# Performance work log

Measured on AMD Instinct MI355X. Metric: run time of the kernel, lower is better.

## Reference

```python
import jax, jax.numpy as jnp
import numpy as np

H = 1024
K = 4  # window_size (causal conv kernel)
HIGHWAY_BIAS = -2.0
SCALE_X = float(np.sqrt(1.0 + np.exp(2.0 * HIGHWAY_BIAS)))  # SRU rescale factor


def _layernorm(x, w, b, eps=1e-5):
    m = jnp.mean(x, axis=-1, keepdims=True)
    v = jnp.mean((x - m) ** 2, axis=-1, keepdims=True)
    return (x - m) * jax.lax.rsqrt(v + eps) * w + b


def _rmsnorm(x, w, eps=1e-6):
    v = jnp.mean(x ** 2, axis=-1, keepdims=True)
    return w * (x * jax.lax.rsqrt(v + eps))


def setup_inputs() -> dict:
    key = jax.random.key(0)
    ks = jax.random.split(key, 12)
    B, L = 8, 4096
    s = 1.0 / np.sqrt(H)
    inp = {
        "x": jax.random.normal(ks[0], (B, L, H), jnp.float32),
        # causal conv1d (full, not depthwise): (out_ch, in_ch, K)
        "conv_w": jax.random.normal(ks[1], (H, H, K), jnp.float32) * (1.0 / np.sqrt(H * K)),
        "conv_b": jnp.zeros((H,), jnp.float32),
        # SRU cell params (k=3 since input_size == hidden_size)
        "sru_ln_w": jnp.ones((H,), jnp.float32),
        "sru_ln_b": jnp.zeros((H,), jnp.float32),
        "sru_W": jax.random.normal(ks[2], (H, 3 * H), jnp.float32) * s,
        "sru_vf": jax.random.normal(ks[3], (H,), jnp.float32) * s,
        "sru_vr": jax.random.normal(ks[4], (H,), jnp.float32) * s,
        "sru_bf": jnp.full((H,), HIGHWAY_BIAS, jnp.float32),
        "sru_br": jnp.zeros((H,), jnp.float32),
        # lambda gate + RMSNorm
        "lambda_w": jax.random.normal(ks[5], (H,), jnp.float32),
        "rms_w": jnp.ones((H,), jnp.float32),
        # FFN token mixer (internal = 2H)
        "ln1_w": jnp.ones((H,), jnp.float32),
        "ln1_b": jnp.zeros((H,), jnp.float32),
        "lin1_w": jax.random.normal(ks[6], (H, 2 * H), jnp.float32) * s,
        "ln2_w": jnp.ones((2 * H,), jnp.float32),
        "ln2_b": jnp.zeros((2 * H,), jnp.float32),
        "lin2_w": jax.random.normal(ks[7], (2 * H, H), jnp.float32) * (1.0 / np.sqrt(2 * H)),
        "lin2_b": jnp.zeros((H,), jnp.float32),
    }
    return inp


def _forward(x, conv_w, conv_b, sru_ln_w, sru_ln_b, sru_W, sru_vf, sru_vr,
             sru_bf, sru_br, lambda_w, rms_w, ln1_w, ln1_b, lin1_w,
             ln2_w, ln2_b, lin2_w, lin2_b):
    B, L, _ = x.shape
    # --- causal conv1d: left-pad K-1, valid conv ---
    xt = jnp.transpose(x, (0, 2, 1))                      # (B, H, L)
    xt = jnp.pad(xt, ((0, 0), (0, 0), (K - 1, 0)))        # (B, H, L+K-1)
    cnn = jax.lax.conv_general_dilated(
        xt, conv_w, window_strides=(1,), padding="VALID",
        dimension_numbers=("NCH", "OIH", "NCH"))          # (B, H, L)
    cnn = cnn + conv_b[None, :, None]
    cnn = jnp.transpose(cnn, (2, 0, 1))                   # (L, B, H)  time-major

    # --- SRU cell (layer_norm=True, use_tanh, rescale) ---
    xn = _layernorm(cnn, sru_ln_w, sru_ln_b)              # (L, B, H)
    U = xn @ sru_W                                        # (L, B, 3H)
    u0, u1, u2 = jnp.split(U, 3, axis=-1)
    xres = xn * SCALE_X

    def step(c, inputs):
        u0t, u1t, u2t, xrt = inputs
        f = jax.nn.sigmoid(u1t + c * sru_vf + sru_bf)
        c_new = f * c + (1.0 - f) * u0t
        r = jax.nn.sigmoid(u2t + c * sru_vr + sru_br)
        h = r * jnp.tanh(c_new) + (1.0 - r) * xrt
        return c_new, h

    c0 = jnp.zeros((B, x.shape[-1]), x.dtype)
    _, hs = jax.lax.scan(step, c0, (u0, u1, u2, xres))    # hs: (L, B, H)

    # --- lambda-gated blend + RMSNorm ---
    out = lambda_w * cnn + (1.0 - lambda_w) * hs          # (L, B, H)
    out = jnp.transpose(out, (1, 0, 2))                   # (B, L, H)
    out = _rmsnorm(out, rms_w)

    # --- block: gate by input, then FFN residual ---
    out = out * x
    t = _layernorm(out, ln1_w, ln1_b)
    t = jax.nn.gelu(t, approximate=False) @ lin1_w        # (B, L, 2H)
    t = _layernorm(t, ln2_w, ln2_b)
    t = jax.nn.gelu(t, approximate=False) @ lin2_w + lin2_b
    return t + out


def reference(x, conv_w, conv_b, sru_ln_w, sru_ln_b, sru_W, sru_vf, sru_vr,
              sru_bf, sru_br, lambda_w, rms_w, ln1_w, ln1_b, lin1_w,
              ln2_w, ln2_b, lin2_w, lin2_b):
    return _forward(x, conv_w, conv_b, sru_ln_w, sru_ln_b, sru_W, sru_vf,
                    sru_vr, sru_bf, sru_br, lambda_w, rms_w, ln1_w, ln1_b,
                    lin1_w, ln2_w, ln2_b, lin2_w, lin2_b)
```

## Files before the change

### kernel.cpp

```cpp
#include <hip/hip_runtime.h>

typedef unsigned short u16;
typedef short bf16x8 __attribute__((ext_vector_type(8)));
typedef float f32x4 __attribute__((ext_vector_type(4)));

#define NTOK 32768
#define LC 512
#define NCH 8
#define MC 8192
#define NFC 4

#define OFF_XB     0ull
#define OFF_CNNB   67108864ull
#define OFF_XNB    134217728ull
#define OFF_U4C    201326592ull
#define OFF_WCT    234881024ull
#define OFF_WSRUT  243269632ull
#define OFF_W1T    249561088ull
#define OFF_W2T    253755392ull
#define OFF_CARRY  257949696ull
#define OFF_P      257982464ull
#define OFF_SCALE  258048000ull
#define OFF_FLAG   258179072ull
#define OFF_ZERO   258179328ull
#define WS_REQ     258183168ull

#define P_CONVB 0
#define P_LNW   1024
#define P_LNB   2048
#define P_VF    3072
#define P_VR    4096
#define P_BF    5120
#define P_BR    6144
#define P_LAM   7168
#define P_RMS   8192
#define P_LN1W  9216
#define P_LN1B  10240
#define P_LIN2B 11264
#define P_LN2W  12288
#define P_LN2B  14336

__device__ __forceinline__ float b2f(u16 u) {
    union { unsigned int i; float f; } v; v.i = ((unsigned int)u) << 16; return v.f;
}
__device__ __forceinline__ u16 f2b(float f) {
    union { float f; unsigned int i; } v; v.f = f;
    unsigned int r = v.i + 0x7fffu + ((v.i >> 16) & 1u);
    return (u16)(r >> 16);
}
__device__ __forceinline__ float ldp(const void* p, size_t i, int fl) {
    return fl ? ((const float*)p)[i] : b2f(((const u16*)p)[i]);
}
__device__ __forceinline__ float gelu_exact(float a) {
    return 0.5f * a * (1.0f + erff(a * 0.70710678118654752f));
}

typedef const __attribute__((address_space(1))) void gas_void;
typedef __attribute__((address_space(3))) void las_void;
__device__ __forceinline__ void gl16(const u16* g, u16* l) {
    __builtin_amdgcn_global_load_lds((gas_void*)g, (las_void*)l, 16, 0, 0);
}

__device__ __forceinline__ int kswz(int row) { return (row + (row >> 3)) & 3; }

__global__ __launch_bounds__(256) void k_fill(float* out, float v) {
    size_t i = ((size_t)blockIdx.x * 256 + threadIdx.x) * 4;
    float4 o; o.x = v; o.y = v; o.z = v; o.w = v;
    *(float4*)(out + i) = o;
}

__global__ void k_detect(const u16* __restrict__ x, int* __restrict__ flag) {
    __shared__ int cnt[4];
    int tid = threadIdx.x;
    int c = 0;
    for (int i = 0; i < 16; ++i) {
        float f = b2f(x[2 * (tid * 16 + i)]);
        if (f != f || fabsf(f) > 1e6f) c++;
    }
    #pragma unroll
    for (int m = 32; m; m >>= 1) c += __shfl_xor(c, m, 64);
    if ((tid & 63) == 0) cnt[tid >> 6] = c;
    __syncthreads();
    if (tid == 0) flag[0] = (cnt[0] + cnt[1] + cnt[2] + cnt[3] > 100) ? 1 : 0;
}

__global__ __launch_bounds__(256) void k_params(const int* __restrict__ flag,
        const void* conv_b, const void* lnw, const void* lnb,
        const void* vf, const void* vr, const void* bf, const void* br,
        const void* lam, const void* rms, const void* ln1w, const void* ln1b,
        const void* lin2b, const void* ln2w, const void* ln2b,
        float* __restrict__ P, float* __restrict__ Z) {
    if (blockIdx.x == 0 && threadIdx.x < 32) Z[threadIdx.x] = 0.0f;
    int idx = blockIdx.x * 256 + threadIdx.x;
    int fl = flag[0];
    int vec = idx >> 10, off = idx & 1023;
    const void* src; size_t so = off;
    switch (vec) {
        case 0: src = conv_b; break;
        case 1: src = lnw; break;
        case 2: src = lnb; break;
        case 3: src = vf; break;
        case 4: src = vr; break;
        case 5: src = bf; break;
        case 6: src = br; break;
        case 7: src = lam; break;
        case 8: src = rms; break;
        case 9: src = ln1w; break;
        case 10: src = ln1b; break;
        case 11: src = lin2b; break;
        case 12: case 13: src = ln2w; so = idx - P_LN2W; break;
        default: src = ln2b; so = idx - P_LN2B; break;
    }
    P[idx] = ldp(src, so, fl);
}

__global__ __launch_bounds__(256) void k_x2b(const int* __restrict__ flag,
                                             const void* __restrict__ x, u16* __restrict__ xb) {
    size_t i = (size_t)blockIdx.x * 256 + threadIdx.x;
    int fl = flag[0];
    ushort4 o;
    if (fl) {
        float4 v = ((const float4*)x)[i];
        o.x = f2b(v.x); o.y = f2b(v.y); o.z = f2b(v.z); o.w = f2b(v.w);
    } else {
        o = ((const ushort4*)x)[i];
    }
    ((ushort4*)xb)[i] = o;
}

__global__ __launch_bounds__(256) void k_conv_reorder(const int* __restrict__ flag,
                                                      const void* __restrict__ w, u16* __restrict__ out) {
    int o = blockIdx.x, fl = flag[0];
    for (int kk = threadIdx.x; kk < 4096; kk += 256) {
        int k = kk >> 10, i = kk & 1023;
        out[(size_t)o * 4096 + kk] = f2b(ldp(w, (size_t)o * 4096 + i * 4 + k, fl));
    }
}

__global__ __launch_bounds__(256) void k_transpose(const int* __restrict__ flag,
                                                   const void* __restrict__ in, u16* __restrict__ out,
                                                   int R, int C) {
    int n = blockIdx.x, fl = flag[0];
    for (int r = threadIdx.x; r < R; r += 256)
        out[(size_t)n * R + r] = f2b(ldp(in, (size_t)r * C + n, fl));
}

template<int MODE, int EPI>
__global__ __launch_bounds__(256) void k_gemm(const u16* __restrict__ A, const u16* __restrict__ Bt,
                                              int N, int K, int nn, int l0, int tok0,
                                              const float* __restrict__ P,
                                              const u16* __restrict__ blend,
                                              const void* __restrict__ xorig,
                                              const float* __restrict__ scale,
                                              const int* __restrict__ flag,
                                              const u16* __restrict__ zb,
                                              void* __restrict__ outp) {
    __shared__ __align__(16) u16 As[128 * 32];
    __shared__ __align__(16) u16 Bs[128 * 32];
    const int tid = threadIdx.x;
    const int lane = tid & 63, wid = tid >> 6;
    const int wm = wid >> 1, wn = wid & 1;

    const int nwg = gridDim.x, bid = blockIdx.x;
    const int q = nwg >> 3, r = nwg & 7;
    const int xcd = bid & 7, idx = bid >> 3;
    const int swz = idx + (xcd < r ? xcd * (q + 1) : r * (q + 1) + (xcd - r) * q);
    const int mi = swz / nn, ni = swz - mi * nn;
    const int m0 = mi << 7, n0 = ni << 7;

    const u16* pa[2]; const u16* pb[2]; int kmin[2];
    u16 *la[2], *lb[2];
    #pragma unroll
    for (int j = 0; j < 2; ++j) {
        int s = tid + j * 256;
        int row = s >> 2;
        int kg = ((s & 3) ^ kswz(row)) << 3;
        la[j] = As + ((s & ~63) << 3);
        lb[j] = Bs + ((s & ~63) << 3);
        pb[j] = Bt + (size_t)(n0 + row) * K + kg;
        kmin[j] = 0;
        if (MODE == 1) {
            int t = m0 + row, b = t >> 12, l = t & 4095;
            pa[j] = A + (((size_t)(b << 12) + (size_t)(l - 3)) << 10) + kg;
            kmin[j] = (3 - l) << 10;
        } else if (MODE == 2) {
            int rg = m0 + row;
            int token = ((rg >> 9) << 12) + l0 + (rg & 511);
            pa[j] = A + ((size_t)token << 10) + kg;
        } else {
            pa[j] = A + (size_t)(m0 + row) * K + kg;
        }
    }

    f32x4 acc[4][4];
    #pragma unroll
    for (int a = 0; a < 4; ++a)
        #pragma unroll
        for (int b = 0; b < 4; ++b)
            #pragma unroll
            for (int rr = 0; rr < 4; ++rr) acc[a][b][rr] = 0.0f;

    int ra[4], rb[4];
    #pragma unroll
    for (int sm = 0; sm < 4; ++sm) {
        int rowa = wm * 64 + sm * 16 + (lane & 15);
        int rowb = wn * 64 + sm * 16 + (lane & 15);
        ra[sm] = (rowa << 5) + ((((lane >> 4) ^ kswz(rowa)) & 3) << 3);
        rb[sm] = (rowb << 5) + ((((lane >> 4) ^ kswz(rowb)) & 3) << 3);
    }

    const int nkb = K >> 5;
    for (int kb = 0; kb < nkb; ++kb) {
        const int k0 = kb << 5;
        __syncthreads();
        #pragma unroll
        for (int j = 0; j < 2; ++j) {
            const u16* ga = pa[j] + k0;
            if (MODE == 1) ga = (k0 < kmin[j]) ? zb : ga;
            gl16(ga, la[j]);
            gl16(pb[j] + k0, lb[j]);
        }
        __syncthreads();

        bf16x8 af[4], bfr[4];
        #pragma unroll
        for (int sm = 0; sm < 4; ++sm) af[sm] = *(const bf16x8*)(As + ra[sm]);
        #pragma unroll
        for (int sn = 0; sn < 4; ++sn) bfr[sn] = *(const bf16x8*)(Bs + rb[sn]);
        #pragma unroll
        for (int sm = 0; sm < 4; ++sm)
            #pragma unroll
            for (int sn = 0; sn < 4; ++sn)
                acc[sm][sn] = __builtin_amdgcn_mfma_f32_16x16x32_bf16(af[sm], bfr[sn], acc[sm][sn], 0, 0, 0);
    }

    int fl = 0;
    if (EPI == 3) fl = flag[0];
    #pragma unroll
    for (int sm = 0; sm < 4; ++sm) {
        #pragma unroll
        for (int sn = 0; sn < 4; ++sn) {
            int rbase = m0 + wm * 64 + sm * 16 + ((lane >> 4) * 4);
            int col   = n0 + wn * 64 + sn * 16 + (lane & 15);
            #pragma unroll
            for (int rr = 0; rr < 4; ++rr) {
                int rowg = rbase + rr;
                float v = acc[sm][sn][rr];
                if (EPI == 0) {
                    ((u16*)outp)[(size_t)rowg * N + col] = f2b(v);
                } else if (EPI == 1) {
                    ((u16*)outp)[(size_t)rowg * N + col] = f2b(v + P[P_CONVB + col]);
                } else {
                    size_t gi = ((size_t)(tok0 + rowg) << 10) + col;
                    float xv = ldp(xorig, gi, fl);
                    float g = b2f(blend[gi]) * scale[tok0 + rowg] * P[P_RMS + col] * xv;
                    float o = v + P[P_LIN2B + col] + g;
                    if (fl) ((float*)outp)[gi] = o;
                    else    ((u16*)outp)[gi] = f2b(o);
                }
            }
        }
    }
}

__device__ __forceinline__ void breduce2(float& a, float& b, volatile float* sa, volatile float* sb, int tid) {
    #pragma unroll
    for (int m = 32; m; m >>= 1) { a += __shfl_xor(a, m, 64); b += __shfl_xor(b, m, 64); }
    int lane = tid & 63, wid = tid >> 6;
    if (lane == 0) { sa[wid] = a; sb[wid] = b; }
    __syncthreads();
    a = sa[0] + sa[1] + sa[2] + sa[3];
    b = sb[0] + sb[1] + sb[2] + sb[3];
    __syncthreads();
}

__global__ __launch_bounds__(256) void k_ln(const u16* __restrict__ cnnb, const float* __restrict__ P,
                                            u16* __restrict__ xnb) {
    __shared__ float sred[8];
    int t = blockIdx.x, tid = threadIdx.x;
    ushort4 cv = ((const ushort4*)(cnnb + ((size_t)t << 10)))[tid];
    float v0 = b2f(cv.x), v1 = b2f(cv.y), v2 = b2f(cv.z), v3 = b2f(cv.w);
    float s = v0 + v1 + v2 + v3;
    float ss = v0 * v0 + v1 * v1 + v2 * v2 + v3 * v3;
    breduce2(s, ss, sred, sred + 4, tid);
    float m = s * (1.0f / 1024.0f);
    float var = ss * (1.0f / 1024.0f) - m * m;
    float rs = rsqrtf(var + 1e-5f);
    int c = tid * 4;
    ushort4 o;
    o.x = f2b((v0 - m) * rs * P[P_LNW + c + 0] + P[P_LNB + c + 0]);
    o.y = f2b((v1 - m) * rs * P[P_LNW + c + 1] + P[P_LNB + c + 1]);
    o.z = f2b((v2 - m) * rs * P[P_LNW + c + 2] + P[P_LNB + c + 2]);
    o.w = f2b((v3 - m) * rs * P[P_LNW + c + 3] + P[P_LNB + c + 3]);
    ((ushort4*)(xnb + ((size_t)t << 10)))[tid] = o;
}

__global__ __launch_bounds__(256) void k_scan(const u16* __restrict__ Uc, const u16* __restrict__ cnnb,
                                              u16* xnblend, float* __restrict__ carry,
                                              const float* __restrict__ P, int l0, int first) {
    int h = blockIdx.x * 256 + threadIdx.x;
    int b = blockIdx.y;
    float vfv = P[P_VF + h], vrv = P[P_VR + h], bfv = P[P_BF + h], brv = P[P_BR + h], lamv = P[P_LAM + h];
    const float SXC = 1.00911627f;
    float c = first ? 0.0f : carry[(b << 10) + h];
    size_t ub = (size_t)b * 512 * 3072 + h;
    size_t gbase = (((size_t)(b * 4096 + l0)) << 10) + h;

    u16 b0[2][8], b1v[2][8], b2v[2][8], bx[2][8], bc[2][8];
    #define SLOAD(g0, s) { \
        _Pragma("unroll") \
        for (int j = 0; j < 8; ++j) { \
            size_t rr = (size_t)((g0) * 8 + j); \
            size_t uo = ub + rr * 3072; \
            b0[s][j] = Uc[uo]; b1v[s][j] = Uc[uo + 1024]; b2v[s][j] = Uc[uo + 2048]; \
            size_t go = gbase + (rr << 10); \
            bx[s][j] = xnblend[go]; bc[s][j] = cnnb[go]; \
        } }
    #define SCOMP(g0, s) { \
        _Pragma("unroll") \
        for (int j = 0; j < 8; ++j) { \
            size_t go = gbase + ((size_t)((g0) * 8 + j) << 10); \
            float u0 = b2f(b0[s][j]), u1 = b2f(b1v[s][j]), u2 = b2f(b2v[s][j]); \
            float xn = b2f(bx[s][j]), cv = b2f(bc[s][j]); \
            float f = 1.0f / (1.0f + __expf(-(u1 + c * vfv + bfv))); \
            float cn = f * (c - u0) + u0; \
            float r_ = 1.0f / (1.0f + __expf(-(u2 + c * vrv + brv))); \
            float e2 = __expf(-2.0f * fabsf(cn)); \
            float th = (1.0f - e2) / (1.0f + e2); \
            th = (cn < 0.0f) ? -th : th; \
            float xr = xn * SXC; \
            float hh = r_ * (th - xr) + xr; \
            xnblend[go] = f2b(lamv * (cv - hh) + hh); \
            c = cn; \
        } }

    SLOAD(0, 0);
    for (int g = 0; g < LC / 8; g += 2) {
        SLOAD(g + 1, 1);
        SCOMP(g, 0);
        if (g + 2 < LC / 8) SLOAD(g + 2, 0);
        SCOMP(g + 1, 1);
    }
    carry[(b << 10) + h] = c;
    #undef SLOAD
    #undef SCOMP
}

__global__ __launch_bounds__(256) void k_rms_ln1(const u16* __restrict__ blend, const void* __restrict__ x,
                                                 const float* __restrict__ P, const int* __restrict__ flag,
                                                 float* __restrict__ scale, u16* __restrict__ A1) {
    __shared__ float sred[8];
    int t = blockIdx.x, tid = threadIdx.x, fl = flag[0];
    ushort4 bv = ((const ushort4*)(blend + ((size_t)t << 10)))[tid];
    float b0 = b2f(bv.x), b1 = b2f(bv.y), b2 = b2f(bv.z), b3 = b2f(bv.w);
    float ss = b0 * b0 + b1 * b1 + b2 * b2 + b3 * b3, dummy = 0.0f;
    breduce2(ss, dummy, sred, sred + 4, tid);
    float sc = rsqrtf(ss * (1.0f / 1024.0f) + 1e-6f);
    if (tid == 0) scale[t] = sc;
    size_t gb = ((size_t)t << 10) + tid * 4;
    int c = tid * 4;
    float g0 = b0 * sc * P[P_RMS + c + 0] * ldp(x, gb + 0, fl);
    float g1 = b1 * sc * P[P_RMS + c + 1] * ldp(x, gb + 1, fl);
    float g2 = b2 * sc * P[P_RMS + c + 2] * ldp(x, gb + 2, fl);
    float g3 = b3 * sc * P[P_RMS + c + 3] * ldp(x, gb + 3, fl);
    float s2 = g0 + g1 + g2 + g3;
    float ss2 = g0 * g0 + g1 * g1 + g2 * g2 + g3 * g3;
    breduce2(s2, ss2, sred, sred + 4, tid);
    float m = s2 * (1.0f / 1024.0f);
    float var = ss2 * (1.0f / 1024.0f) - m * m;
    float rs = rsqrtf(var + 1e-5f);
    ushort4 o;
    o.x = f2b(gelu_exact((g0 - m) * rs * P[P_LN1W + c + 0] + P[P_LN1B + c + 0]));
    o.y = f2b(gelu_exact((g1 - m) * rs * P[P_LN1W + c + 1] + P[P_LN1B + c + 1]));
    o.z = f2b(gelu_exact((g2 - m) * rs * P[P_LN1W + c + 2] + P[P_LN1B + c + 2]));
    o.w = f2b(gelu_exact((g3 - m) * rs * P[P_LN1W + c + 3] + P[P_LN1B + c + 3]));
    ((ushort4*)(A1 + ((size_t)t << 10)))[tid] = o;
}

__global__ __launch_bounds__(256) void k_ln2_gelu(const u16* __restrict__ T1c, const float* __restrict__ P,
                                                  u16* __restrict__ A2c) {
    __shared__ float sred[8];
    int t = blockIdx.x, tid = threadIdx.x;
    const ushort4* tp = (const ushort4*)(T1c + ((size_t)t << 11));
    ushort4 va = tp[tid * 2], vb = tp[tid * 2 + 1];
    float e[8] = { b2f(va.x), b2f(va.y), b2f(va.z), b2f(va.w),
                   b2f(vb.x), b2f(vb.y), b2f(vb.z), b2f(vb.w) };
    float s = 0.0f, ss = 0.0f;
    #pragma unroll
    for (int i = 0; i < 8; ++i) { s += e[i]; ss += e[i] * e[i]; }
    breduce2(s, ss, sred, sred + 4, tid);
    float m = s * (1.0f / 2048.0f);
    float var = ss * (1.0f / 2048.0f) - m * m;
    float rs = rsqrtf(var + 1e-5f);
    int c = tid * 8;
    u16 oo[8];
    #pragma unroll
    for (int i = 0; i < 8; ++i)
        oo[i] = f2b(gelu_exact((e[i] - m) * rs * P[P_LN2W + c + i] + P[P_LN2B + c + i]));
    ushort4 oa, ob;
    oa.x = oo[0]; oa.y = oo[1]; oa.z = oo[2]; oa.w = oo[3];
    ob.x = oo[4]; ob.y = oo[5]; ob.z = oo[6]; ob.w = oo[7];
    ushort4* op = (ushort4*)(A2c + ((size_t)t << 11));
    op[tid * 2] = oa; op[tid * 2 + 1] = ob;
}

extern "C" void kernel_launch(void* const* d_in, const int* in_sizes, int n_in,
                              void* d_out, int out_size, void* d_ws, size_t ws_size,
                              hipStream_t stream) {
    (void)in_sizes; (void)n_in; (void)out_size;
    const void* x        = d_in[0];
    const void* conv_w   = d_in[1];
    const void* conv_b   = d_in[2];
    const void* sru_ln_w = d_in[3];
    const void* sru_ln_b = d_in[4];
    const void* sru_W    = d_in[5];
    const void* sru_vf   = d_in[6];
    const void* sru_vr   = d_in[7];
    const void* sru_bf   = d_in[8];
    const void* sru_br   = d_in[9];
    const void* lambda_w = d_in[10];
    const void* rms_w    = d_in[11];
    const void* ln1_w    = d_in[12];
    const void* ln1_b    = d_in[13];
    const void* lin1_w   = d_in[14];
    const void* ln2_w    = d_in[15];
    const void* ln2_b    = d_in[16];
    const void* lin2_w   = d_in[17];
    const void* lin2_b   = d_in[18];

    if (ws_size < WS_REQ) {
        float sv = 1000.0f + (float)(ws_size >> 20);
        k_fill<<<16384, 256, 0, stream>>>((float*)d_out, sv);
        return;
    }

    char* ws = (char*)d_ws;
    u16*   xb    = (u16*)(ws + OFF_XB);
    u16*   cnnb  = (u16*)(ws + OFF_CNNB);
    u16*   xnb   = (u16*)(ws + OFF_XNB);
    u16*   Uc    = (u16*)(ws + OFF_U4C);
    u16*   WcT   = (u16*)(ws + OFF_WCT);
    u16*   WsruT = (u16*)(ws + OFF_WSRUT);
    u16*   W1T   = (u16*)(ws + OFF_W1T);
    u16*   W2T   = (u16*)(ws + OFF_W2T);
    float* carry = (float*)(ws + OFF_CARRY);
    float* P     = (float*)(ws + OFF_P);
    float* scale = (float*)(ws + OFF_SCALE);
    int*   flag  = (int*)(ws + OFF_FLAG);
    float* zbuf  = (float*)(ws + OFF_ZERO);
    const u16* zb16 = (const u16*)zbuf;
    u16*   A1  = xb;
    u16*   T1c = cnnb;
    u16*   A2c = (u16*)(ws + OFF_CNNB + 33554432);

    k_detect<<<1, 256, 0, stream>>>((const u16*)x, flag);
    k_params<<<64, 256, 0, stream>>>(flag, conv_b, sru_ln_w, sru_ln_b, sru_vf, sru_vr,
                                     sru_bf, sru_br, lambda_w, rms_w, ln1_w, ln1_b,
                                     lin2_b, ln2_w, ln2_b, P, zbuf);
    k_x2b<<<32768, 256, 0, stream>>>(flag, x, xb);
    k_conv_reorder<<<1024, 256, 0, stream>>>(flag, conv_w, WcT);
    k_gemm<1, 1><<<2048, 256, 0, stream>>>(xb, WcT, 1024, 4096, 8, 0, 0,
                                           P, nullptr, nullptr, nullptr, flag, zb16, cnnb);
    k_ln<<<32768, 256, 0, stream>>>(cnnb, P, xnb);
    k_transpose<<<3072, 256, 0, stream>>>(flag, sru_W, WsruT, 1024, 3072);
    for (int ch = 0; ch < NCH; ++ch) {
        int l0 = ch * LC;
        k_gemm<2, 0><<<768, 256, 0, stream>>>(xnb, WsruT, 3072, 1024, 24, l0, 0,
                                              P, nullptr, nullptr, nullptr, flag, zb16, Uc);
        k_scan<<<dim3(4, 8), 256, 0, stream>>>(Uc, cnnb, xnb, carry, P, l0, ch == 0);
    }
    k_rms_ln1<<<32768, 256, 0, stream>>>(xnb, x, P, flag, scale, A1);
    k_transpose<<<2048, 256, 0, stream>>>(flag, lin1_w, W1T, 1024, 2048);
    k_transpose<<<1024, 256, 0, stream>>>(flag, lin2_w, W2T, 2048, 1024);
    for (int c = 0; c < NFC; ++c) {
        int tok0 = c * MC;
        k_gemm<0, 0><<<1024, 256, 0, stream>>>(A1 + ((size_t)tok0 << 10), W1T, 2048, 1024, 16, 0, 0,
                                               P, nullptr, nullptr, nullptr, flag, zb16, T1c);
        k_ln2_gelu<<<MC, 256, 0, stream>>>(T1c, P, A2c);
        k_gemm<0, 3><<<512, 256, 0, stream>>>(A2c, W2T, 1024, 2048, 8, 0, tok0,
                                              P, xnb, x, scale, flag, zb16, d_out);
    }
}
```

Baseline: 3.013 ms.

## Interleave SRU gate output by 8 timesteps and spread scan across more blocks

The SRU projection GEMM gets a new epilogue that writes its output in a layout where 8 consecutive timesteps of each gate and channel are contiguous. This lets the scan load them as one 16-byte vector instead of 24 scalar strided loads. The scan now uses 64-thread blocks (128 blocks instead of 32) with triple-buffered prefetch, and the chunk length doubles to 1024 so there are half as many GEMM/scan launch pairs. The U buffer is moved to reuse the xb region, and the scattered ushort4 stores in the GEMM epilogue may be less coalesced.

```diff
diff --git a/kernel.cpp b/kernel.cpp
--- a/kernel.cpp
+++ b/kernel.cpp
@@ -3,10 +3,12 @@
 typedef unsigned short u16;
 typedef short bf16x8 __attribute__((ext_vector_type(8)));
 typedef float f32x4 __attribute__((ext_vector_type(4)));
+typedef unsigned short u16x8 __attribute__((ext_vector_type(8)));
 
 #define NTOK 32768
-#define LC 512
-#define NCH 8
+#define LC 1024
+#define L2LC 10
+#define NCH 4
 #define MC 8192
 #define NFC 4
 
@@ -185,7 +187,7 @@
             kmin[j] = (3 - l) << 10;
         } else if (MODE == 2) {
             int rg = m0 + row;
-            int token = ((rg >> 9) << 12) + l0 + (rg & 511);
+            int token = ((rg >> L2LC) << 12) + l0 + (rg & (LC - 1));
             pa[j] = A + ((size_t)token << 10) + kg;
         } else {
             pa[j] = A + (size_t)(m0 + row) * K + kg;
@@ -242,21 +244,31 @@
         for (int sn = 0; sn < 4; ++sn) {
             int rbase = m0 + wm * 64 + sm * 16 + ((lane >> 4) * 4);
             int col   = n0 + wn * 64 + sn * 16 + (lane & 15);
-            #pragma unroll
-            for (int rr = 0; rr < 4; ++rr) {
-                int rowg = rbase + rr;
-                float v = acc[sm][sn][rr];
-                if (EPI == 0) {
-                    ((u16*)outp)[(size_t)rowg * N + col] = f2b(v);
-                } else if (EPI == 1) {
-                    ((u16*)outp)[(size_t)rowg * N + col] = f2b(v + P[P_CONVB + col]);
-                } else {
-                    size_t gi = ((size_t)(tok0 + rowg) << 10) + col;
-                    float xv = ldp(xorig, gi, fl);
-                    float g = b2f(blend[gi]) * scale[tok0 + rowg] * P[P_RMS + col] * xv;
-                    float o = v + P[P_LIN2B + col] + g;
-                    if (fl) ((float*)outp)[gi] = o;
-                    else    ((u16*)outp)[gi] = f2b(o);
+            if (EPI == 2) {
+                int bI = rbase >> L2LC, rloc = rbase & (LC - 1);
+                int p = col >> 10, hh = col & 1023;
+                size_t idx8 = ((((size_t)(bI * 3 + p) * (LC / 8)) + (rloc >> 3)) << 10) + hh;
+                ushort4 o4;
+                o4.x = f2b(acc[sm][sn][0]); o4.y = f2b(acc[sm][sn][1]);
+                o4.z = f2b(acc[sm][sn][2]); o4.w = f2b(acc[sm][sn][3]);
+                *(ushort4*)((u16*)outp + (idx8 << 3) + (rloc & 7)) = o4;
+            } else {
+                #pragma unroll
+                for (int rr = 0; rr < 4; ++rr) {
+                    int rowg = rbase + rr;
+                    float v = acc[sm][sn][rr];
+                    if (EPI == 0) {
+                        ((u16*)outp)[(size_t)rowg * N + col] = f2b(v);
+                    } else if (EPI == 1) {
+                        ((u16*)outp)[(size_t)rowg * N + col] = f2b(v + P[P_CONVB + col]);
+                    } else {
+                        size_t gi = ((size_t)(tok0 + rowg) << 10) + col;
+                        float xv = ldp(xorig, gi, fl);
+                        float g = b2f(blend[gi]) * scale[tok0 + rowg] * P[P_RMS + col] * xv;
+                        float o = v + P[P_LIN2B + col] + g;
+                        if (fl) ((float*)outp)[gi] = o;
+                        else    ((u16*)outp)[gi] = f2b(o);
+                    }
                 }
             }
         }
@@ -295,32 +307,37 @@
     ((ushort4*)(xnb + ((size_t)t << 10)))[tid] = o;
 }
 
-__global__ __launch_bounds__(256) void k_scan(const u16* __restrict__ Uc, const u16* __restrict__ cnnb,
-                                              u16* xnblend, float* __restrict__ carry,
-                                              const float* __restrict__ P, int l0, int first) {
-    int h = blockIdx.x * 256 + threadIdx.x;
+__global__ __launch_bounds__(64) void k_scan(const u16* __restrict__ Uc, const u16* __restrict__ cnnb,
+                                             u16* xnblend, float* __restrict__ carry,
+                                             const float* __restrict__ P, int l0, int first) {
+    int h = blockIdx.x * 64 + threadIdx.x;
     int b = blockIdx.y;
     float vfv = P[P_VF + h], vrv = P[P_VR + h], bfv = P[P_BF + h], brv = P[P_BR + h], lamv = P[P_LAM + h];
     const float SXC = 1.00911627f;
     float c = first ? 0.0f : carry[(b << 10) + h];
-    size_t ub = (size_t)b * 512 * 3072 + h;
+    const u16x8* U8 = (const u16x8*)Uc;
+    size_t u0b = (((size_t)(b * 3 + 0) * (LC / 8)) << 10) + h;
+    size_t u1b = (((size_t)(b * 3 + 1) * (LC / 8)) << 10) + h;
+    size_t u2b = (((size_t)(b * 3 + 2) * (LC / 8)) << 10) + h;
     size_t gbase = (((size_t)(b * 4096 + l0)) << 10) + h;
 
-    u16 b0[2][8], b1v[2][8], b2v[2][8], bx[2][8], bc[2][8];
+    u16x8 a0[3], a1[3], a2[3];
+    u16 bx[3][8], bc[3][8];
     #define SLOAD(g0, s) { \
+        size_t gg = (size_t)(g0); \
+        a0[s] = U8[u0b + (gg << 10)]; \
+        a1[s] = U8[u1b + (gg << 10)]; \
+        a2[s] = U8[u2b + (gg << 10)]; \
         _Pragma("unroll") \
         for (int j = 0; j < 8; ++j) { \
-            size_t rr = (size_t)((g0) * 8 + j); \
-            size_t uo = ub + rr * 3072; \
-            b0[s][j] = Uc[uo]; b1v[s][j] = Uc[uo + 1024]; b2v[s][j] = Uc[uo + 2048]; \
-            size_t go = gbase + (rr << 10); \
+            size_t go = gbase + ((gg * 8 + j) << 10); \
             bx[s][j] = xnblend[go]; bc[s][j] = cnnb[go]; \
         } }
     #define SCOMP(g0, s) { \
         _Pragma("unroll") \
         for (int j = 0; j < 8; ++j) { \
-            size_t go = gbase + ((size_t)((g0) * 8 + j) << 10); \
-            float u0 = b2f(b0[s][j]), u1 = b2f(b1v[s][j]), u2 = b2f(b2v[s][j]); \
+            size_t go = gbase + (((size_t)(g0) * 8 + j) << 10); \
+            float u0 = b2f(a0[s][j]), u1 = b2f(a1[s][j]), u2 = b2f(a2[s][j]); \
             float xn = b2f(bx[s][j]), cv = b2f(bc[s][j]); \
             float f = 1.0f / (1.0f + __expf(-(u1 + c * vfv + bfv))); \
             float cn = f * (c - u0) + u0; \
@@ -334,12 +351,17 @@
             c = cn; \
         } }
 
+    const int G = LC / 8;
     SLOAD(0, 0);
-    for (int g = 0; g < LC / 8; g += 2) {
-        SLOAD(g + 1, 1);
+    SLOAD(1, 1);
+    #pragma unroll 1
+    for (int g = 0; g < G; g += 3) {
+        if (g + 2 < G) SLOAD(g + 2, 2);
         SCOMP(g, 0);
-        if (g + 2 < LC / 8) SLOAD(g + 2, 0);
-        SCOMP(g + 1, 1);
+        if (g + 3 < G) SLOAD(g + 3, 0);
+        if (g + 1 < G) SCOMP(g + 1, 1);
+        if (g + 4 < G) SLOAD(g + 4, 1);
+        if (g + 2 < G) SCOMP(g + 2, 2);
     }
     carry[(b << 10) + h] = c;
     #undef SLOAD
@@ -438,7 +460,7 @@
     u16*   xb    = (u16*)(ws + OFF_XB);
     u16*   cnnb  = (u16*)(ws + OFF_CNNB);
     u16*   xnb   = (u16*)(ws + OFF_XNB);
-    u16*   Uc    = (u16*)(ws + OFF_U4C);
+    u16*   Uc    = (u16*)(ws + OFF_XB);
     u16*   WcT   = (u16*)(ws + OFF_WCT);
     u16*   WsruT = (u16*)(ws + OFF_WSRUT);
     u16*   W1T   = (u16*)(ws + OFF_W1T);
@@ -465,9 +487,9 @@
     k_transpose<<<3072, 256, 0, stream>>>(flag, sru_W, WsruT, 1024, 3072);
     for (int ch = 0; ch < NCH; ++ch) {
         int l0 = ch * LC;
-        k_gemm<2, 0><<<768, 256, 0, stream>>>(xnb, WsruT, 3072, 1024, 24, l0, 0,
-                                              P, nullptr, nullptr, nullptr, flag, zb16, Uc);
-        k_scan<<<dim3(4, 8), 256, 0, stream>>>(Uc, cnnb, xnb, carry, P, l0, ch == 0);
+        k_gemm<2, 2><<<1536, 256, 0, stream>>>(xnb, WsruT, 3072, 1024, 24, l0, 0,
+                                               P, nullptr, nullptr, nullptr, flag, zb16, Uc);
+        k_scan<<<dim3(16, 8), 64, 0, stream>>>(Uc, cnnb, xnb, carry, P, l0, ch == 0);
     }
     k_rms_ln1<<<32768, 256, 0, stream>>>(xnb, x, P, flag, scale, A1);
     k_transpose<<<2048, 256, 0, stream>>>(flag, lin1_w, W1T, 1024, 2048);
```

After: 2.827 ms. 1.07x faster.
